# Performance work log

Hardware: AMD Instinct MI355X
Metric: run time of the kernel (lower is better)

Reference implementation:

```python
import jax, jax.numpy as jnp
import numpy as np

WS = 7            # window_size
P = WS * WS       # tokens per window
NUM_HEADS = 12
N_SCALES = 3      # n_local_region_scales
LOCAL_HEAD = NUM_HEADS // N_SCALES

# relative position index (Swin-style), precomputed as a constant
_coords = np.stack(np.meshgrid(np.arange(WS), np.arange(WS), indexing='ij'))  # (2,WS,WS)
_cf = _coords.reshape(2, -1)                                                  # (2,P)
_rel = (_cf[:, :, None] - _cf[:, None, :]).transpose(1, 2, 0)                 # (P,P,2)
_rel[:, :, 0] += WS - 1
_rel[:, :, 1] += WS - 1
_rel[:, :, 0] *= 2 * WS - 1
REL_IDX = jnp.asarray(_rel.sum(-1))  # (P,P) int


def window_partition(arr, ws):
    # arr: (B, H, W, C) -> (B * H/ws * W/ws, ws, ws, C)
    B, H, W, C = arr.shape
    a = arr.reshape(B, H // ws, ws, W // ws, ws, C)
    return a.transpose(0, 1, 3, 2, 4, 5).reshape(-1, ws, ws, C)


def setup_inputs() -> dict:
    key = jax.random.key(0)
    ks = jax.random.split(key, 4)
    B, H, W, C = 16, 56, 56, 384
    N = H * W
    return {
        'x': jax.random.normal(ks[0], (B, N, C), dtype=jnp.float32),
        'w_qkv': jax.random.normal(ks[1], (C, 3 * C), dtype=jnp.float32) * 0.02,
        'w_proj': jax.random.normal(ks[2], (C, C), dtype=jnp.float32) * 0.02,
        'b_proj': jnp.zeros((C,), dtype=jnp.float32),
        'rel_bias_table': jax.random.normal(ks[3], ((2 * WS - 1) ** 2, LOCAL_HEAD), dtype=jnp.float32) * 0.02,
        'H': H,
        'W': W,
    }


def reference(x, w_qkv, w_proj, b_proj, rel_bias_table, H, W):
    B, N, C = x.shape
    head_dim = C // NUM_HEADS
    local_C = C // N_SCALES
    scale = head_dim ** -0.5

    # qkv projection (no bias), laid out as (3, B, N, C)
    temp = (x @ w_qkv).reshape(B, N, 3, C).transpose(2, 0, 1, 3)

    # relative position bias: (LOCAL_HEAD, P, P)
    bias = rel_bias_table[REL_IDX.reshape(-1)].reshape(P, P, LOCAL_HEAD).transpose(2, 0, 1)

    outs = []
    for i in range(N_SCALES):
        qkv = temp[:, :, :, i * local_C:(i + 1) * local_C]          # (3,B,N,local_C)
        oh, ow = H // (2 ** i), W // (2 ** i)
        n_region = (oh // WS) * (ow // WS)
        qkv = qkv.reshape(3 * B, N, local_C).transpose(0, 2, 1).reshape(3 * B, local_C, H, W)
        if i > 0:
            k = 2 ** i
            r = qkv.reshape(3 * B, local_C, oh, k, ow, k)
            qkv = r.mean(axis=(3, 5)) + r.max(axis=(3, 5))           # avg_pool + max_pool
        qkv = qkv.transpose(0, 2, 3, 1)                              # (3B, oh, ow, local_C)
        qkv = window_partition(qkv, WS)                              # (3B*n_region, WS, WS, local_C)
        qkv = qkv.reshape(3, B, n_region, WS, WS, LOCAL_HEAD, head_dim).transpose(0, 1, 5, 2, 3, 4, 6)
        # NOTE: the original reshapes (B,LOCAL_HEAD,n_region,WS,WS,hd) -> (-1,LOCAL_HEAD,P,hd),
        # which mixes batch/head/region axes; replicated faithfully (row-major reshape).
        q = qkv[0].reshape(-1, LOCAL_HEAD, P, head_dim)
        kk = qkv[1].reshape(-1, LOCAL_HEAD, P, head_dim)
        v = qkv[2].reshape(-1, LOCAL_HEAD, P, head_dim)
        attn = (q * scale) @ jnp.swapaxes(kk, -2, -1) + bias[None]   # (B*R, LH, P, P)
        attn = jax.nn.softmax(attn, axis=-1)
        y = attn @ v                                                 # (B*R, LH, P, hd)
        # faithful inverse of the mixed reshape + (non-inverse) window merge via plain reshape
        y = y.reshape(B, n_region, LOCAL_HEAD, P, head_dim).transpose(0, 2, 4, 1, 3)
        y = y.reshape(B, local_C, oh, ow)
        if i > 0:
            y = jax.image.resize(y, (B, local_C, H, W), method='bilinear')
        y = y.reshape(B, LOCAL_HEAD, head_dim, H, W).transpose(0, 1, 3, 4, 2)  # (B,LH,H,W,hd)
        outs.append(y)

    fused = jnp.concatenate(outs, axis=1)                            # (B,NUM_HEADS,H,W,hd)
    fused = fused.reshape(B, NUM_HEADS, N, C // NUM_HEADS).transpose(0, 2, 1, 3).reshape(B, N, C)
    return fused @ w_proj + b_proj
```

## Files before the change

kernel.cpp:

```cpp
#include <hip/hip_runtime.h>
#include <hip/hip_bf16.h>

typedef __hip_bfloat16 bf16;
typedef __hip_bfloat162 bf16x2;
typedef __attribute__((ext_vector_type(8))) short short8;
typedef __attribute__((ext_vector_type(4))) float f32x4;

__device__ __forceinline__ void storeOut(float* p, float v) { *p = v; }
__device__ __forceinline__ void storeOut(bf16* p, float v) { *p = __float2bfloat16(v); }

#define GLOAD_LDS16(g, l)                                              \
  __builtin_amdgcn_global_load_lds(                                    \
      (const __attribute__((address_space(1))) void*)(g),              \
      (__attribute__((address_space(3))) void*)(l), 16, 0, 0)

__global__ __launch_bounds__(256) void prep_kernel(const float* __restrict__ x,
                                                   const float* __restrict__ w_qkv,
                                                   const float* __restrict__ w_proj,
                                                   bf16* __restrict__ xb,
                                                   bf16* __restrict__ wqkvT,
                                                   bf16* __restrict__ wprojT)
{
  int bid = blockIdx.x;
  if (bid < 9408) {
    int i = bid * 256 + threadIdx.x;
    const float4* p = (const float4*)x + (size_t)i * 2;
    float4 a = p[0], b = p[1];
    union { short8 v; bf16 h[8]; } u;
    u.h[0] = __float2bfloat16(a.x); u.h[1] = __float2bfloat16(a.y);
    u.h[2] = __float2bfloat16(a.z); u.h[3] = __float2bfloat16(a.w);
    u.h[4] = __float2bfloat16(b.x); u.h[5] = __float2bfloat16(b.y);
    u.h[6] = __float2bfloat16(b.z); u.h[7] = __float2bfloat16(b.w);
    *((short8*)xb + i) = u.v;
  } else {
    int idx = (bid - 9408) * 256 + threadIdx.x;
    if (idx < 1152 * 384) {
      int n = idx / 384, k = idx - n * 384;
      wqkvT[idx] = __float2bfloat16(w_qkv[(size_t)k * 1152 + n]);
    } else {
      idx -= 1152 * 384;
      int n = idx / 384, k = idx - n * 384;
      wprojT[idx] = __float2bfloat16(w_proj[(size_t)k * 384 + n]);
    }
  }
}

template<typename TC, bool BIAS>
__global__ __launch_bounds__(512) void gemm_mfma(const bf16* __restrict__ A,
                                                 const bf16* __restrict__ Bt,
                                                 const float* __restrict__ bias,
                                                 TC* __restrict__ C,
                                                 int M, int N, int K, int nbx)
{
  __shared__ __align__(16) bf16 As[256 * 64];
  __shared__ __align__(16) bf16 Bs[128 * 64];
  const int tid = threadIdx.x;
  const int wave = tid >> 6, lane = tid & 63;
  const int nwg = gridDim.x;
  const int qc = nwg >> 3, rr = nwg & 7;
  const int xcd = blockIdx.x & 7, jj = blockIdx.x >> 3;
  const int wg = (xcd < rr ? xcd * (qc + 1) : rr * (qc + 1) + (xcd - rr) * qc) + jj;
  const int by = wg / nbx, bx = wg - by * nbx;
  const int bm = by * 256, bn = bx * 128;
  const int wr = wave >> 1, wc = wave & 1;

  f32x4 acc[4][4] = {};

  const bf16* aP[4];
  const bf16* bP[2];
#pragma unroll
  for (int e = 0; e < 4; ++e) {
    int flat = e * 8192 + tid * 16;
    int r = flat >> 7;
    int q = ((flat >> 4) & 7) ^ (r & 7);
    aP[e] = A + (size_t)(bm + r) * K + q * 8;
  }
#pragma unroll
  for (int e = 0; e < 2; ++e) {
    int flat = e * 8192 + tid * 16;
    int r = flat >> 7;
    int q = ((flat >> 4) & 7) ^ (r & 7);
    bP[e] = Bt + (size_t)(bn + r) * K + q * 8;
  }
  char* AsW = (char*)As + wave * 1024;
  char* BsW = (char*)Bs + wave * 1024;

  const int lr = lane & 15, lk = lane >> 4;
  const int rbA = (wr * 64 + lr) * 64;
  const int rbB = (wc * 64 + lr) * 64;
  const int q0 = ((lk    ) ^ (lr & 7)) * 8;
  const int q1 = ((4 + lk) ^ (lr & 7)) * 8;

  for (int k0 = 0; k0 < K; k0 += 64) {
#pragma unroll
    for (int e = 0; e < 4; ++e) GLOAD_LDS16(aP[e] + k0, AsW + e * 8192);
#pragma unroll
    for (int e = 0; e < 2; ++e) GLOAD_LDS16(bP[e] + k0, BsW + e * 8192);
    __syncthreads();
    short8 af0[4], af1[4], bf0[4], bf1[4];
#pragma unroll
    for (int i = 0; i < 4; ++i) {
      af0[i] = *(const short8*)(As + rbA + i * 1024 + q0);
      af1[i] = *(const short8*)(As + rbA + i * 1024 + q1);
    }
#pragma unroll
    for (int j = 0; j < 4; ++j) {
      bf0[j] = *(const short8*)(Bs + rbB + j * 1024 + q0);
      bf1[j] = *(const short8*)(Bs + rbB + j * 1024 + q1);
    }
#pragma unroll
    for (int i = 0; i < 4; ++i)
#pragma unroll
      for (int j = 0; j < 4; ++j) {
        acc[i][j] = __builtin_amdgcn_mfma_f32_16x16x32_bf16(af0[i], bf0[j], acc[i][j], 0, 0, 0);
        acc[i][j] = __builtin_amdgcn_mfma_f32_16x16x32_bf16(af1[i], bf1[j], acc[i][j], 0, 0, 0);
      }
    __syncthreads();
  }

  const int crow = bm + wr * 64 + lk * 4;
  const int ccol = bn + wc * 64 + lr;
#pragma unroll
  for (int j = 0; j < 4; ++j) {
    int col = ccol + j * 16;
    float bv = BIAS ? bias[col] : 0.f;
#pragma unroll
    for (int i = 0; i < 4; ++i)
#pragma unroll
      for (int t = 0; t < 4; ++t) {
        int row = crow + i * 16 + t;
        storeOut(&C[(size_t)row * N + col], acc[i][j][t] + bv);
      }
  }
}

__global__ __launch_bounds__(128) void pool_both_kernel(const bf16* __restrict__ temp,
                                                        bf16* __restrict__ pool1,
                                                        bf16* __restrict__ pool2)
{
  int blk = blockIdx.x;
  bf16* outp; int oh, k, isc;
  if (blk < 3 * 16 * 28 * 28) { outp = pool1; oh = 28; k = 2; isc = 1; }
  else { blk -= 3 * 16 * 28 * 28; outp = pool2; oh = 14; k = 4; isc = 2; }
  const int ow = oh;
  int c = threadIdx.x;
  int x = blk % ow; int t = blk / ow;
  int y = t % oh;  t /= oh;
  int b = t % 16;  int s = t / 16;
  float sum = 0.f, mx = -3.4e38f;
  float inv = 1.0f / (float)(k * k);
  for (int dy = 0; dy < k; ++dy)
    for (int dx = 0; dx < k; ++dx) {
      int h = y * k + dy, w = x * k + dx;
      float v = __bfloat162float(temp[((size_t)b * 3136 + h * 56 + w) * 1152 + s * 384 + isc * 128 + c]);
      sum += v; mx = fmaxf(mx, v);
    }
  outp[((size_t)(s * 16 + b) * oh * ow + y * ow + x) * 128 + c] = __float2bfloat16(sum * inv + mx);
}

struct AttnP {
  const bf16 *qb, *kb, *vb;
  bf16* out;
  int R, Rw, ow, npos, rstride, out_cstride, out_coffset, blk0;
  long long bstride;
};

__global__ __launch_bounds__(256) void attn_mfma(const float* __restrict__ btable,
                                                 AttnP P0, AttnP P1, AttnP P2)
{
  __shared__ __align__(16) bf16 KP[4 * 4096];
  __shared__ __align__(16) bf16 Vt[4 * 2048];
  __shared__ float bias_s[169];

  const AttnP p = (blockIdx.x >= (unsigned)P2.blk0) ? P2
                : (blockIdx.x >= (unsigned)P1.blk0) ? P1 : P0;
  const int blk = blockIdx.x - p.blk0;
  const int b = blk / p.R, r = blk % p.R;
  const int rh = r / p.Rw, rw = r % p.Rw;
  const int tid = threadIdx.x;
  const int h = tid >> 6, lane = tid & 63;
  const int lr = lane & 15, lk = lane >> 4;
  const int hb = r & 3;

  if (tid < 169) bias_s[tid] = btable[tid * 4 + hb];

  const size_t gbase = (size_t)b * p.bstride;

  for (int c = tid; c < 784; c += 256) {
    int hh = c / 196, rem = c - hh * 196;
    int row = rem >> 2, slot = rem & 3;
    int r7 = (row * 9363) >> 16, rm = row - r7 * 7;
    int n = (rh * 7 + r7) * p.ow + rw * 7 + rm;
    short8 v = *(const short8*)(p.kb + gbase + (size_t)n * p.rstride + hh * 32 + slot * 8);
    *(short8*)(KP + hh * 4096 + row * 40 + slot * 8) = v;
  }
  for (int j = tid; j < 4096; j += 256) {
    int pp = j & 63, dp = (j >> 6) & 15, hh = j >> 10;
    bf16 v0, v1;
    if (pp < 49) {
      int r7 = (pp * 9363) >> 16, rm = pp - r7 * 7;
      int n = (rh * 7 + r7) * p.ow + rw * 7 + rm;
      bf16x2 v2 = *(const bf16x2*)(p.vb + gbase + (size_t)n * p.rstride + hh * 32 + dp * 2);
      v0 = v2.x; v1 = v2.y;
    } else { v0 = __float2bfloat16(0.f); v1 = v0; }
    int d0 = dp * 2, d1 = d0 + 1;
    Vt[hh * 2048 + d0 * 64 + ((pp >> 3) ^ (d0 & 7)) * 8 + (pp & 7)] = v0;
    Vt[hh * 2048 + d1 * 64 + ((pp >> 3) ^ (d1 & 7)) * 8 + (pp & 7)] = v1;
  }

  short8 qa[4];
#pragma unroll
  for (int it = 0; it < 4; ++it) {
    int pq = it * 16 + lr; pq = min(pq, 48);
    int r7 = (pq * 9363) >> 16, rm = pq - r7 * 7;
    int n = (rh * 7 + r7) * p.ow + rw * 7 + rm;
    qa[it] = *(const short8*)(p.qb + gbase + (size_t)n * p.rstride + h * 32 + lk * 8);
  }

  __syncthreads();

  f32x4 s[4][4];
  {
    short8 kf[4];
#pragma unroll
    for (int jt = 0; jt < 4; ++jt)
      kf[jt] = *(const short8*)(KP + h * 4096 + (jt * 16 + lr) * 40 + lk * 8);
    const f32x4 z = {0.f, 0.f, 0.f, 0.f};
    __builtin_amdgcn_s_setprio(1);
#pragma unroll
    for (int it = 0; it < 4; ++it)
#pragma unroll
      for (int jt = 0; jt < 4; ++jt)
        s[it][jt] = __builtin_amdgcn_mfma_f32_16x16x32_bf16(qa[it], kf[jt], z, 0, 0, 0);
    __builtin_amdgcn_s_setprio(0);
  }

  const float scale = 0.17677669529663687f;
  const bool colpad = (lr != 0);
  int pp7[4], ppm[4];
#pragma unroll
  for (int jt = 0; jt < 4; ++jt) {
    int pp = min(jt * 16 + lr, 48);
    pp7[jt] = (pp * 9363) >> 16; ppm[jt] = pp - pp7[jt] * 7;
  }
  float sm[4][4];
#pragma unroll
  for (int it = 0; it < 4; ++it)
#pragma unroll
    for (int t = 0; t < 4; ++t) {
      int pq = min(it * 16 + lk * 4 + t, 48);
      int q7 = (pq * 9363) >> 16, qm = pq - q7 * 7;
#pragma unroll
      for (int jt = 0; jt < 4; ++jt) {
        float bv = bias_s[(q7 - pp7[jt] + 6) * 13 + (qm - ppm[jt] + 6)];
        float v = fmaf(s[it][jt][t], scale, bv);
        if (jt == 3 && colpad) v = -1e30f;
        s[it][jt][t] = v;
      }
      float m = fmaxf(fmaxf(s[it][0][t], s[it][1][t]), fmaxf(s[it][2][t], s[it][3][t]));
      m = fmaxf(m, __shfl_xor(m, 1));
      m = fmaxf(m, __shfl_xor(m, 2));
      m = fmaxf(m, __shfl_xor(m, 4));
      m = fmaxf(m, __shfl_xor(m, 8));
      float ssum = 0.f;
#pragma unroll
      for (int jt = 0; jt < 4; ++jt) {
        float e = __expf(s[it][jt][t] - m);
        s[it][jt][t] = e; ssum += e;
      }
      ssum += __shfl_xor(ssum, 1);
      ssum += __shfl_xor(ssum, 2);
      ssum += __shfl_xor(ssum, 4);
      ssum += __shfl_xor(ssum, 8);
      sm[it][t] = 1.0f / ssum;
    }

#pragma unroll
  for (int it = 0; it < 4; ++it)
#pragma unroll
    for (int t = 0; t < 4; ++t) {
      int prow = it * 16 + lk * 4 + t;
#pragma unroll
      for (int jt = 0; jt < 4; ++jt) {
        int slot = (jt * 2 + (lr >> 3)) ^ (prow & 7);
        KP[h * 4096 + prow * 64 + slot * 8 + (lr & 7)] = __float2bfloat16(s[it][jt][t]);
      }
    }
  __syncthreads();

  f32x4 o[4][2] = {};
#pragma unroll
  for (int ks = 0; ks < 2; ++ks) {
    short8 pf[4], vf[2];
#pragma unroll
    for (int it = 0; it < 4; ++it) {
      int prow = it * 16 + lr;
      pf[it] = *(const short8*)(KP + h * 4096 + prow * 64 + ((ks * 4 + lk) ^ (prow & 7)) * 8);
    }
#pragma unroll
    for (int jd = 0; jd < 2; ++jd) {
      int d = jd * 16 + lr;
      vf[jd] = *(const short8*)(Vt + h * 2048 + d * 64 + ((ks * 4 + lk) ^ (d & 7)) * 8);
    }
    __builtin_amdgcn_s_setprio(1);
#pragma unroll
    for (int it = 0; it < 4; ++it)
#pragma unroll
      for (int jd = 0; jd < 2; ++jd)
        o[it][jd] = __builtin_amdgcn_mfma_f32_16x16x32_bf16(pf[it], vf[jd], o[it][jd], 0, 0, 0);
    __builtin_amdgcn_s_setprio(0);
  }

  const int c0 = (r & 3) * 32;
#pragma unroll
  for (int it = 0; it < 4; ++it)
#pragma unroll
    for (int t = 0; t < 4; ++t) {
      int prow = it * 16 + lk * 4 + t;
      if (prow < 49) {
        int m_out = (h * (p.R >> 2) + (r >> 2)) * 49 + prow;
        bf16* op = p.out + ((size_t)b * p.npos + m_out) * p.out_cstride + p.out_coffset + c0;
#pragma unroll
        for (int jd = 0; jd < 2; ++jd)
          op[jd * 16 + lr] = __float2bfloat16(o[it][jd][t] * sm[it][t]);
      }
    }
}

__device__ __forceinline__ float2 bilerp2(const bf16* __restrict__ base, int dim, int h, int w, int cp)
{
  float r = (float)dim / 56.f;
  float uy = (h + 0.5f) * r - 0.5f;
  float ux = (w + 0.5f) * r - 0.5f;
  float fy0 = floorf(uy), fx0 = floorf(ux);
  int y0 = (int)fy0, x0 = (int)fx0;
  float fy = uy - fy0, fx = ux - fx0;
  int y0c = max(y0, 0), y1c = min(y0 + 1, dim - 1);
  int x0c = max(x0, 0), x1c = min(x0 + 1, dim - 1);
  bf16x2 v00 = *(const bf16x2*)(base + ((size_t)y0c * dim + x0c) * 128 + cp * 2);
  bf16x2 v01 = *(const bf16x2*)(base + ((size_t)y0c * dim + x1c) * 128 + cp * 2);
  bf16x2 v10 = *(const bf16x2*)(base + ((size_t)y1c * dim + x0c) * 128 + cp * 2);
  bf16x2 v11 = *(const bf16x2*)(base + ((size_t)y1c * dim + x1c) * 128 + cp * 2);
  float w00 = (1.f - fy) * (1.f - fx), w01 = (1.f - fy) * fx;
  float w10 = fy * (1.f - fx),        w11 = fy * fx;
  float2 o;
  o.x = w00 * __bfloat162float(v00.x) + w01 * __bfloat162float(v01.x) +
        w10 * __bfloat162float(v10.x) + w11 * __bfloat162float(v11.x);
  o.y = w00 * __bfloat162float(v00.y) + w01 * __bfloat162float(v01.y) +
        w10 * __bfloat162float(v10.y) + w11 * __bfloat162float(v11.y);
  return o;
}

__global__ __launch_bounds__(256) void upsample_both_kernel(const bf16* __restrict__ yb1,
                                                            const bf16* __restrict__ yb2,
                                                            bf16* __restrict__ fused)
{
  int t = blockIdx.x * 256 + threadIdx.x;
  int cp = t & 63;
  int pos = t >> 6;
  int n = pos % 3136, b = pos / 3136;
  int h = n / 56, w = n % 56;
  float2 s1 = bilerp2(yb1 + (size_t)b * 784 * 128, 28, h, w, cp);
  float2 s2 = bilerp2(yb2 + (size_t)b * 196 * 128, 14, h, w, cp);
  bf16* op = fused + (size_t)pos * 384;
  bf16x2 o1; o1.x = __float2bfloat16(s1.x); o1.y = __float2bfloat16(s1.y);
  bf16x2 o2; o2.x = __float2bfloat16(s2.x); o2.y = __float2bfloat16(s2.y);
  *(bf16x2*)(op + 128 + cp * 2) = o1;
  *(bf16x2*)(op + 256 + cp * 2) = o2;
}

extern "C" void kernel_launch(void* const* d_in, const int* in_sizes, int n_in,
                              void* d_out, int out_size, void* d_ws, size_t ws_size,
                              hipStream_t stream)
{
  const float* x      = (const float*)d_in[0];
  const float* w_qkv  = (const float*)d_in[1];
  const float* w_proj = (const float*)d_in[2];
  const float* b_proj = (const float*)d_in[3];
  const float* btable = (const float*)d_in[4];

  bf16* temp  = (bf16*)d_ws;
  bf16* pool1 = temp  + (size_t)50176 * 1152;
  bf16* pool2 = pool1 + (size_t)3 * 16 * 784 * 128;
  bf16* fused = pool2 + (size_t)3 * 16 * 196 * 128;
  bf16* ybuf1 = fused + (size_t)50176 * 384;
  bf16* ybuf2 = ybuf1 + (size_t)16 * 784 * 128;
  bf16* wqkvT = ybuf2 + (size_t)16 * 196 * 128;
  bf16* wprojT= wqkvT + (size_t)1152 * 384;
  bf16* xb    = fused;

  prep_kernel<<<9408 + 2304, 256, 0, stream>>>(x, w_qkv, w_proj, xb, wqkvT, wprojT);

  gemm_mfma<bf16, false><<<1764, 512, 0, stream>>>(
      xb, wqkvT, nullptr, temp, 50176, 1152, 384, 9);

  pool_both_kernel<<<3 * 16 * 28 * 28 + 3 * 16 * 14 * 14, 128, 0, stream>>>(temp, pool1, pool2);

  AttnP P0{temp, temp + 384, temp + 768, fused,
           64, 8, 56, 3136, 1152, 384, 0, 0, (long long)3136 * 1152};
  AttnP P1{pool1, pool1 + (size_t)16 * 784 * 128, pool1 + (size_t)2 * 16 * 784 * 128, ybuf1,
           16, 4, 28, 784, 128, 128, 0, 1024, (long long)784 * 128};
  AttnP P2{pool2, pool2 + (size_t)16 * 196 * 128, pool2 + (size_t)2 * 16 * 196 * 128, ybuf2,
           4, 2, 14, 196, 128, 128, 0, 1280, (long long)196 * 128};
  attn_mfma<<<1344, 256, 0, stream>>>(btable, P0, P1, P2);

  upsample_both_kernel<<<16 * 3136 * 64 / 256, 256, 0, stream>>>(ybuf1, ybuf2, fused);

  gemm_mfma<float, true><<<588, 512, 0, stream>>>(
      fused, wprojT, b_proj, (float*)d_out, 50176, 384, 384, 3);
}
```

Measured before the change: 205.0 us.

## Double-buffer GEMM LDS tiles with K-step 32 to overlap loads and MFMA

```diff
diff --git a/kernel.cpp b/kernel.cpp
--- a/kernel.cpp
+++ b/kernel.cpp
@@ -52,8 +52,8 @@
                                                  TC* __restrict__ C,
                                                  int M, int N, int K, int nbx)
 {
-  __shared__ __align__(16) bf16 As[256 * 64];
-  __shared__ __align__(16) bf16 Bs[128 * 64];
+  __shared__ __align__(16) bf16 As[2][256 * 32];
+  __shared__ __align__(16) bf16 Bs[2][128 * 32];
   const int tid = threadIdx.x;
   const int wave = tid >> 6, lane = tid & 63;
   const int nwg = gridDim.x;
@@ -66,56 +66,55 @@
 
   f32x4 acc[4][4] = {};
 
-  const bf16* aP[4];
-  const bf16* bP[2];
-#pragma unroll
-  for (int e = 0; e < 4; ++e) {
-    int flat = e * 8192 + tid * 16;
-    int r = flat >> 7;
-    int q = ((flat >> 4) & 7) ^ (r & 7);
-    aP[e] = A + (size_t)(bm + r) * K + q * 8;
-  }
+  const bf16* aP[2];
+  const bf16* bP0;
 #pragma unroll
   for (int e = 0; e < 2; ++e) {
     int flat = e * 8192 + tid * 16;
-    int r = flat >> 7;
-    int q = ((flat >> 4) & 7) ^ (r & 7);
-    bP[e] = Bt + (size_t)(bn + r) * K + q * 8;
-  }
-  char* AsW = (char*)As + wave * 1024;
-  char* BsW = (char*)Bs + wave * 1024;
+    int r = flat >> 6;
+    int q = ((flat >> 4) & 3) ^ ((r >> 1) & 3);
+    aP[e] = A + (size_t)(bm + r) * K + q * 8;
+  }
+  {
+    int flat = tid * 16;
+    int r = flat >> 6;
+    int q = ((flat >> 4) & 3) ^ ((r >> 1) & 3);
+    bP0 = Bt + (size_t)(bn + r) * K + q * 8;
+  }
+
+  auto STAGE = [&](int buf, int k0) {
+    char* aw = (char*)(&As[buf][0]) + wave * 1024;
+    char* bw = (char*)(&Bs[buf][0]) + wave * 1024;
+    GLOAD_LDS16(aP[0] + k0, aw);
+    GLOAD_LDS16(aP[1] + k0, aw + 8192);
+    GLOAD_LDS16(bP0 + k0, bw);
+  };
 
   const int lr = lane & 15, lk = lane >> 4;
-  const int rbA = (wr * 64 + lr) * 64;
-  const int rbB = (wc * 64 + lr) * 64;
-  const int q0 = ((lk    ) ^ (lr & 7)) * 8;
-  const int q1 = ((4 + lk) ^ (lr & 7)) * 8;
-
-  for (int k0 = 0; k0 < K; k0 += 64) {
-#pragma unroll
-    for (int e = 0; e < 4; ++e) GLOAD_LDS16(aP[e] + k0, AsW + e * 8192);
-#pragma unroll
-    for (int e = 0; e < 2; ++e) GLOAD_LDS16(bP[e] + k0, BsW + e * 8192);
+  const int rbA = (wr * 64 + lr) * 32;
+  const int rbB = (wc * 64 + lr) * 32;
+  const int qx = (lk ^ ((lr >> 1) & 3)) * 8;
+
+  const int nt = K >> 5;
+  STAGE(0, 0);
+  __syncthreads();
+  int cur = 0;
+  for (int t = 0; t < nt; ++t) {
+    if (t + 1 < nt) STAGE(cur ^ 1, (t + 1) << 5);
+    const bf16* Ab = &As[cur][0];
+    const bf16* Bb = &Bs[cur][0];
+    short8 af[4], bfr[4];
+#pragma unroll
+    for (int i = 0; i < 4; ++i) af[i]  = *(const short8*)(Ab + rbA + i * 512 + qx);
+#pragma unroll
+    for (int j = 0; j < 4; ++j) bfr[j] = *(const short8*)(Bb + rbB + j * 512 + qx);
+#pragma unroll
+    for (int i = 0; i < 4; ++i)
+#pragma unroll
+      for (int j = 0; j < 4; ++j)
+        acc[i][j] = __builtin_amdgcn_mfma_f32_16x16x32_bf16(af[i], bfr[j], acc[i][j], 0, 0, 0);
     __syncthreads();
-    short8 af0[4], af1[4], bf0[4], bf1[4];
-#pragma unroll
-    for (int i = 0; i < 4; ++i) {
-      af0[i] = *(const short8*)(As + rbA + i * 1024 + q0);
-      af1[i] = *(const short8*)(As + rbA + i * 1024 + q1);
-    }
-#pragma unroll
-    for (int j = 0; j < 4; ++j) {
-      bf0[j] = *(const short8*)(Bs + rbB + j * 1024 + q0);
-      bf1[j] = *(const short8*)(Bs + rbB + j * 1024 + q1);
-    }
-#pragma unroll
-    for (int i = 0; i < 4; ++i)
-#pragma unroll
-      for (int j = 0; j < 4; ++j) {
-        acc[i][j] = __builtin_amdgcn_mfma_f32_16x16x32_bf16(af0[i], bf0[j], acc[i][j], 0, 0, 0);
-        acc[i][j] = __builtin_amdgcn_mfma_f32_16x16x32_bf16(af1[i], bf1[j], acc[i][j], 0, 0, 0);
-      }
-    __syncthreads();
+    cur ^= 1;
   }
 
   const int crow = bm + wr * 64 + lk * 4;
```

Measured after the change: 211.7 us. +3.3%, slower.

## Fuse avg+max pooling into attention loads and schedule coarse scales first

Applied to the files above, without the earlier changes.

```diff
diff --git a/kernel.cpp b/kernel.cpp
--- a/kernel.cpp
+++ b/kernel.cpp
@@ -6,6 +6,9 @@
 typedef __attribute__((ext_vector_type(8))) short short8;
 typedef __attribute__((ext_vector_type(4))) float f32x4;
 
+__device__ __forceinline__ float bf2f(short v) {
+  return __uint_as_float(((unsigned)(unsigned short)v) << 16);
+}
 __device__ __forceinline__ void storeOut(float* p, float v) { *p = v; }
 __device__ __forceinline__ void storeOut(bf16* p, float v) { *p = __float2bfloat16(v); }
 
@@ -134,35 +137,10 @@
   }
 }
 
-__global__ __launch_bounds__(128) void pool_both_kernel(const bf16* __restrict__ temp,
-                                                        bf16* __restrict__ pool1,
-                                                        bf16* __restrict__ pool2)
-{
-  int blk = blockIdx.x;
-  bf16* outp; int oh, k, isc;
-  if (blk < 3 * 16 * 28 * 28) { outp = pool1; oh = 28; k = 2; isc = 1; }
-  else { blk -= 3 * 16 * 28 * 28; outp = pool2; oh = 14; k = 4; isc = 2; }
-  const int ow = oh;
-  int c = threadIdx.x;
-  int x = blk % ow; int t = blk / ow;
-  int y = t % oh;  t /= oh;
-  int b = t % 16;  int s = t / 16;
-  float sum = 0.f, mx = -3.4e38f;
-  float inv = 1.0f / (float)(k * k);
-  for (int dy = 0; dy < k; ++dy)
-    for (int dx = 0; dx < k; ++dx) {
-      int h = y * k + dy, w = x * k + dx;
-      float v = __bfloat162float(temp[((size_t)b * 3136 + h * 56 + w) * 1152 + s * 384 + isc * 128 + c]);
-      sum += v; mx = fmaxf(mx, v);
-    }
-  outp[((size_t)(s * 16 + b) * oh * ow + y * ow + x) * 128 + c] = __float2bfloat16(sum * inv + mx);
-}
-
 struct AttnP {
   const bf16 *qb, *kb, *vb;
   bf16* out;
-  int R, Rw, ow, npos, rstride, out_cstride, out_coffset, blk0;
-  long long bstride;
+  int R, Rw, f, npos, out_cstride, out_coffset, blk0;
 };
 
 __global__ __launch_bounds__(256) void attn_mfma(const float* __restrict__ btable,
@@ -172,8 +150,8 @@
   __shared__ __align__(16) bf16 Vt[4 * 2048];
   __shared__ float bias_s[169];
 
-  const AttnP p = (blockIdx.x >= (unsigned)P2.blk0) ? P2
-                : (blockIdx.x >= (unsigned)P1.blk0) ? P1 : P0;
+  const AttnP p = (blockIdx.x >= (unsigned)P0.blk0) ? P0
+                : (blockIdx.x >= (unsigned)P1.blk0) ? P1 : P2;
   const int blk = blockIdx.x - p.blk0;
   const int b = blk / p.R, r = blk % p.R;
   const int rh = r / p.Rw, rw = r % p.Rw;
@@ -181,31 +159,77 @@
   const int h = tid >> 6, lane = tid & 63;
   const int lr = lane & 15, lk = lane >> 4;
   const int hb = r & 3;
+  const int f = p.f;
+  const float pinv = 1.0f / (float)(f * f);
 
   if (tid < 169) bias_s[tid] = btable[tid * 4 + hb];
 
-  const size_t gbase = (size_t)b * p.bstride;
+  const size_t gbase = (size_t)b * 3136 * 1152;
 
   for (int c = tid; c < 784; c += 256) {
     int hh = c / 196, rem = c - hh * 196;
     int row = rem >> 2, slot = rem & 3;
     int r7 = (row * 9363) >> 16, rm = row - r7 * 7;
-    int n = (rh * 7 + r7) * p.ow + rw * 7 + rm;
-    short8 v = *(const short8*)(p.kb + gbase + (size_t)n * p.rstride + hh * 32 + slot * 8);
-    *(short8*)(KP + hh * 4096 + row * 40 + slot * 8) = v;
-  }
-  for (int j = tid; j < 4096; j += 256) {
-    int pp = j & 63, dp = (j >> 6) & 15, hh = j >> 10;
-    bf16 v0, v1;
+    const bf16* src = p.kb + gbase +
+        ((size_t)((rh * 7 + r7) * f) * 56 + (rw * 7 + rm) * f) * 1152 + hh * 32 + slot * 8;
+    short8 ov;
+    if (f == 1) {
+      ov = *(const short8*)src;
+    } else {
+      float sum[8] = {}, mx[8];
+#pragma unroll
+      for (int e = 0; e < 8; ++e) mx[e] = -3.4e38f;
+      for (int dy = 0; dy < f; ++dy)
+        for (int dx = 0; dx < f; ++dx) {
+          short8 v = *(const short8*)(src + ((size_t)dy * 56 + dx) * 1152);
+#pragma unroll
+          for (int e = 0; e < 8; ++e) {
+            float fv = bf2f(v[e]); sum[e] += fv; mx[e] = fmaxf(mx[e], fv);
+          }
+        }
+      union { short8 v; bf16 hh2[8]; } u;
+#pragma unroll
+      for (int e = 0; e < 8; ++e) u.hh2[e] = __float2bfloat16(sum[e] * pinv + mx[e]);
+      ov = u.v;
+    }
+    *(short8*)(KP + hh * 4096 + row * 40 + slot * 8) = ov;
+  }
+
+  for (int j = tid; j < 1024; j += 256) {
+    int pp = j & 63, d8 = (j >> 6) & 3, hh = j >> 8;
+    bf16 hv[8];
     if (pp < 49) {
       int r7 = (pp * 9363) >> 16, rm = pp - r7 * 7;
-      int n = (rh * 7 + r7) * p.ow + rw * 7 + rm;
-      bf16x2 v2 = *(const bf16x2*)(p.vb + gbase + (size_t)n * p.rstride + hh * 32 + dp * 2);
-      v0 = v2.x; v1 = v2.y;
-    } else { v0 = __float2bfloat16(0.f); v1 = v0; }
-    int d0 = dp * 2, d1 = d0 + 1;
-    Vt[hh * 2048 + d0 * 64 + ((pp >> 3) ^ (d0 & 7)) * 8 + (pp & 7)] = v0;
-    Vt[hh * 2048 + d1 * 64 + ((pp >> 3) ^ (d1 & 7)) * 8 + (pp & 7)] = v1;
+      const bf16* src = p.vb + gbase +
+          ((size_t)((rh * 7 + r7) * f) * 56 + (rw * 7 + rm) * f) * 1152 + hh * 32 + d8 * 8;
+      if (f == 1) {
+        short8 v = *(const short8*)src;
+#pragma unroll
+        for (int e = 0; e < 8; ++e) { unsigned short bb = (unsigned short)v[e]; hv[e] = *(bf16*)&bb; }
+      } else {
+        float sum[8] = {}, mx[8];
+#pragma unroll
+        for (int e = 0; e < 8; ++e) mx[e] = -3.4e38f;
+        for (int dy = 0; dy < f; ++dy)
+          for (int dx = 0; dx < f; ++dx) {
+            short8 v = *(const short8*)(src + ((size_t)dy * 56 + dx) * 1152);
+#pragma unroll
+            for (int e = 0; e < 8; ++e) {
+              float fv = bf2f(v[e]); sum[e] += fv; mx[e] = fmaxf(mx[e], fv);
+            }
+          }
+#pragma unroll
+        for (int e = 0; e < 8; ++e) hv[e] = __float2bfloat16(sum[e] * pinv + mx[e]);
+      }
+    } else {
+#pragma unroll
+      for (int e = 0; e < 8; ++e) hv[e] = __float2bfloat16(0.f);
+    }
+#pragma unroll
+    for (int e = 0; e < 8; ++e) {
+      int d = d8 * 8 + e;
+      Vt[hh * 2048 + d * 64 + ((pp >> 3) ^ (d & 7)) * 8 + (pp & 7)] = hv[e];
+    }
   }
 
   short8 qa[4];
@@ -213,8 +237,27 @@
   for (int it = 0; it < 4; ++it) {
     int pq = it * 16 + lr; pq = min(pq, 48);
     int r7 = (pq * 9363) >> 16, rm = pq - r7 * 7;
-    int n = (rh * 7 + r7) * p.ow + rw * 7 + rm;
-    qa[it] = *(const short8*)(p.qb + gbase + (size_t)n * p.rstride + h * 32 + lk * 8);
+    const bf16* src = p.qb + gbase +
+        ((size_t)((rh * 7 + r7) * f) * 56 + (rw * 7 + rm) * f) * 1152 + h * 32 + lk * 8;
+    if (f == 1) {
+      qa[it] = *(const short8*)src;
+    } else {
+      float sum[8] = {}, mx[8];
+#pragma unroll
+      for (int e = 0; e < 8; ++e) mx[e] = -3.4e38f;
+      for (int dy = 0; dy < f; ++dy)
+        for (int dx = 0; dx < f; ++dx) {
+          short8 v = *(const short8*)(src + ((size_t)dy * 56 + dx) * 1152);
+#pragma unroll
+          for (int e = 0; e < 8; ++e) {
+            float fv = bf2f(v[e]); sum[e] += fv; mx[e] = fmaxf(mx[e], fv);
+          }
+        }
+      union { short8 v; bf16 hh2[8]; } u;
+#pragma unroll
+      for (int e = 0; e < 8; ++e) u.hh2[e] = __float2bfloat16(sum[e] * pinv + mx[e]);
+      qa[it] = u.v;
+    }
   }
 
   __syncthreads();
@@ -380,9 +423,7 @@
   const float* btable = (const float*)d_in[4];
 
   bf16* temp  = (bf16*)d_ws;
-  bf16* pool1 = temp  + (size_t)50176 * 1152;
-  bf16* pool2 = pool1 + (size_t)3 * 16 * 784 * 128;
-  bf16* fused = pool2 + (size_t)3 * 16 * 196 * 128;
+  bf16* fused = temp  + (size_t)50176 * 1152 + (size_t)3 * 16 * 980 * 128;
   bf16* ybuf1 = fused + (size_t)50176 * 384;
   bf16* ybuf2 = ybuf1 + (size_t)16 * 784 * 128;
   bf16* wqkvT = ybuf2 + (size_t)16 * 196 * 128;
@@ -394,14 +435,12 @@
   gemm_mfma<bf16, false><<<1764, 512, 0, stream>>>(
       xb, wqkvT, nullptr, temp, 50176, 1152, 384, 9);
 
-  pool_both_kernel<<<3 * 16 * 28 * 28 + 3 * 16 * 14 * 14, 128, 0, stream>>>(temp, pool1, pool2);
-
+  AttnP P2{temp + 256, temp + 640, temp + 1024, ybuf2,
+           4, 2, 4, 196, 128, 0, 0};
+  AttnP P1{temp + 128, temp + 512, temp + 896, ybuf1,
+           16, 4, 2, 784, 128, 0, 64};
   AttnP P0{temp, temp + 384, temp + 768, fused,
-           64, 8, 56, 3136, 1152, 384, 0, 0, (long long)3136 * 1152};
-  AttnP P1{pool1, pool1 + (size_t)16 * 784 * 128, pool1 + (size_t)2 * 16 * 784 * 128, ybuf1,
-           16, 4, 28, 784, 128, 128, 0, 1024, (long long)784 * 128};
-  AttnP P2{pool2, pool2 + (size_t)16 * 196 * 128, pool2 + (size_t)2 * 16 * 196 * 128, ybuf2,
-           4, 2, 14, 196, 128, 128, 0, 1280, (long long)196 * 128};
+           64, 8, 1, 3136, 384, 0, 320};
   attn_mfma<<<1344, 256, 0, stream>>>(btable, P0, P1, P2);
 
   upsample_both_kernel<<<16 * 3136 * 64 / 256, 256, 0, stream>>>(ybuf1, ybuf2, fused);
```

New measurement: 204.9 us. About the same (-0.0%).
